# Kernel optimization log

Hardware: AMD Instinct MI355X
Metric: run time of the kernel (lower is better)

Reference implementation:

```python
import jax, jax.numpy as jnp
import numpy as np
from jax import lax

EPS = 1e-5

def quantize_ternary(w):
    # scale = mean(|w|).clamp_min(1e-5) computed on detached weight
    scale = jnp.maximum(jnp.mean(jnp.abs(lax.stop_gradient(w))), EPS)
    ws = w / scale
    # STE: forward uses round+clamp, backward is identity in ws
    wq = lax.stop_gradient(jnp.clip(jnp.round(ws), -1.0, 1.0) - ws) + ws
    return wq * scale

def conv2d(x, w, b):
    # x: [N,C,H,W], w: [O,I,kh,kw], stride 1, pad 1 -> same spatial size
    out = lax.conv_general_dilated(
        x, w, window_strides=(1, 1), padding=[(1, 1), (1, 1)],
        dimension_numbers=("NCHW", "OIHW", "NCHW"))
    return out + b[None, :, None, None]

def setup_inputs() -> dict:
    key = jax.random.key(0)
    k1, k2, k3, k4, k5 = jax.random.split(key, 5)
    N, C_in, C_out, H, W, K = 16, 64, 64, 128, 128, 3
    fan_in = C_in * K * K
    bound = 1.0 / np.sqrt(fan_in)
    x = jax.random.normal(k1, (N, C_in, H, W), dtype=jnp.float32)
    w = jax.random.uniform(k2, (C_out, C_in, K, K), minval=-bound, maxval=bound, dtype=jnp.float32)
    b = jax.random.uniform(k3, (C_out,), minval=-bound, maxval=bound, dtype=jnp.float32)
    # growth child: kaiming-uniform-like init scaled by 0.01, zero bias
    w_child = jax.random.uniform(k4, (C_out, C_in, K, K), minval=-bound, maxval=bound, dtype=jnp.float32) * 0.01
    b_child = jnp.zeros((C_out,), dtype=jnp.float32)
    gate = jnp.zeros((1,), dtype=jnp.float32)  # growth_gate buffer
    return {"x": x, "w": w, "b": b, "w_child": w_child, "b_child": b_child, "gate": gate}

def reference(x, w, b, w_child, b_child, gate):
    out = conv2d(x, quantize_ternary(w), b)
    child_out = conv2d(x, quantize_ternary(w_child), b_child)
    g = jax.nn.sigmoid(gate)  # shape [1], broadcasts
    return out + g * child_out
```

## Files before the change

### kernel.cpp

```cpp
#include <hip/hip_runtime.h>
#include <math.h>


typedef __attribute__((ext_vector_type(8))) short short8;
typedef __attribute__((ext_vector_type(4))) float float4v;

__device__ inline unsigned short f2bf(float f) {
  union { float f; unsigned u; } v; v.f = f;
  unsigned u = v.u;
  return (unsigned short)((u + 0x7FFFu + ((u >> 16) & 1u)) >> 16);
}

__global__ __launch_bounds__(1024) void reduce_abs_part(const float* __restrict__ w,
                                                        const float* __restrict__ wc,
                                                        double* __restrict__ part) {
  const int base = blockIdx.x * 4096 + threadIdx.x;
  double a = 0.0, c = 0.0;
#pragma unroll
  for (int i = 0; i < 4; ++i) {
    a += (double)fabsf(w[base + i * 1024]);
    c += (double)fabsf(wc[base + i * 1024]);
  }
#pragma unroll
  for (int off = 32; off > 0; off >>= 1) {
    a += __shfl_down(a, off);
    c += __shfl_down(c, off);
  }
  __shared__ double sa[16], sc[16];
  int wv = threadIdx.x >> 6;
  if ((threadIdx.x & 63) == 0) { sa[wv] = a; sc[wv] = c; }
  __syncthreads();
  if (threadIdx.x == 0) {
    double ta = 0.0, tc = 0.0;
#pragma unroll
    for (int i = 0; i < 16; ++i) { ta += sa[i]; tc += sc[i]; }
    part[blockIdx.x] = ta;
    part[9 + blockIdx.x] = tc;
  }
}

__global__ void quant_combine(const float* __restrict__ w, const float* __restrict__ wc,
                              const float* __restrict__ b, const float* __restrict__ bc,
                              const float* __restrict__ gate, const double* __restrict__ part,
                              unsigned short* __restrict__ wq, float* __restrict__ beff) {
  double s0 = 0.0, s1 = 0.0;
#pragma unroll
  for (int i = 0; i < 9; ++i) { s0 += part[i]; s1 += part[9 + i]; }
  const float sw = fmaxf((float)(s0 * (1.0 / 36864.0)), 1e-5f);
  const float sc = fmaxf((float)(s1 * (1.0 / 36864.0)), 1e-5f);
  const float g = 1.0f / (1.0f + expf(-gate[0]));
  int idx = blockIdx.x * 256 + threadIdx.x;
  int tap = idx >> 12;
  int oc = (idx >> 6) & 63;
  int ci = idx & 63;
  int src = oc * 576 + ci * 9 + tap;
  float q1 = fminf(1.f, fmaxf(-1.f, rintf(w[src] / sw))) * sw;
  float q2 = fminf(1.f, fmaxf(-1.f, rintf(wc[src] / sc))) * sc;
  wq[idx] = f2bf(q1 + g * q2);
  if (idx < 64) beff[idx] = b[idx] + g * bc[idx];
}

__global__ __launch_bounds__(512, 2) void conv_fused(
    const float* __restrict__ x, const unsigned short* __restrict__ wq,
    const float* __restrict__ beff, float* __restrict__ out) {
  extern __shared__ __align__(16) char smem[];
  char* Abase = smem;
  char* Bbase = smem + 99200;

  const int bid = blockIdx.x;
  const int xcd = bid & 7;
  const int u = bid >> 3;
  const int n = xcd * 2 + (u >> 5);
  const int h0 = (u & 31) * 4;
  const int tid = threadIdx.x;
  const int lane = tid & 63;
  const int wv = tid >> 6;
  const int rw = wv >> 1;
  const int pxh = (wv & 1) * 64;
  const int ln15 = lane & 15;
  const int lq = lane >> 4;

  const float* xn = x + (size_t)n * (64 * 16384);

  const short8 b0v = *(const short8*)(wq + tid * 8);

  if (tid < 56) {
    int slot = (tid < 48) ? ((tid >> 3) * 129 * 8 + (tid & 7)) : (6192 + (tid - 48));
    *(short8*)(Abase + (slot << 4)) = (short8)0;
  }

  const int w128 = tid & 127;
  const int hi = tid >> 7;
#pragma unroll 4
  for (int pass = 0; pass < 12; ++pass) {
    const int k = pass * 4 + hi;
    const int r = k >> 3;
    const int c = k & 7;
    const int h = h0 + r - 1;
    short8 v = (short8)0;
    if ((unsigned)h < 128u) {
      const float* sp = xn + c * 8 * 16384 + h * 128 + w128;
      v[0] = (short)f2bf(sp[0 * 16384]);
      v[1] = (short)f2bf(sp[1 * 16384]);
      v[2] = (short)f2bf(sp[2 * 16384]);
      v[3] = (short)f2bf(sp[3 * 16384]);
      v[4] = (short)f2bf(sp[4 * 16384]);
      v[5] = (short)f2bf(sp[5 * 16384]);
      v[6] = (short)f2bf(sp[6 * 16384]);
      v[7] = (short)f2bf(sp[7 * 16384]);
    }
    const int p = w128 + 1;
    const int slot = (r * 129 + p) * 8 + (c ^ (p & 7));
    *(short8*)(Abase + (slot << 4)) = v;
  }

  const int bslot = (tid & ~7) | ((tid & 7) ^ ((tid >> 3) & 7));
  *(short8*)(Bbase + (bslot << 4)) = b0v;
  __syncthreads();

  float4v acc[4][4] = {};

#pragma unroll
  for (int tap = 0; tap < 9; ++tap) {
    const int cb = tap & 1;
    short8 btrans;
    if (tap < 8) btrans = *(const short8*)(wq + (tap + 1) * 4096 + tid * 8);

    const int dh = tap / 3;
    const int dw = tap - dh * 3;
    const int r = rw + dh;
    const int pb = pxh + ln15 + dw;
    const int a0 = (((r * 129 + pb) << 3) + (lq ^ (pb & 7))) << 4;
    short8 Ab[2][4], Bb[2][4];
#pragma unroll
    for (int mf = 0; mf < 4; ++mf) {
      Ab[0][mf] = *(const short8*)(Abase + (a0 + mf * 2048));
      Ab[1][mf] = *(const short8*)(Abase + ((a0 ^ 64) + mf * 2048));
    }
#pragma unroll
    for (int qd = 0; qd < 4; ++qd) {
      const int oc = qd * 16 + ln15;
      Bb[0][qd] = *(const short8*)(Bbase + cb * 8192 +
                                   ((oc * 8 + (lq ^ (ln15 & 7))) << 4));
      Bb[1][qd] = *(const short8*)(Bbase + cb * 8192 +
                                   ((oc * 8 + ((lq + 4) ^ (ln15 & 7))) << 4));
    }

    __builtin_amdgcn_s_setprio(1);
#pragma unroll
    for (int cc2 = 0; cc2 < 2; ++cc2)
#pragma unroll
      for (int mf = 0; mf < 4; ++mf)
#pragma unroll
        for (int qd = 0; qd < 4; ++qd)
          acc[mf][qd] = __builtin_amdgcn_mfma_f32_16x16x32_bf16(
              Ab[cc2][mf], Bb[cc2][qd], acc[mf][qd], 0, 0, 0);
    __builtin_amdgcn_s_setprio(0);

    if (tap < 8) {
      *(short8*)(Bbase + (cb ^ 1) * 8192 + (bslot << 4)) = btrans;
      __syncthreads();
    }
  }

  const int rq = lane >> 4;
  float bias[4];
#pragma unroll
  for (int q = 0; q < 4; ++q) bias[q] = beff[q * 16 + ln15];
#pragma unroll
  for (int mf = 0; mf < 4; ++mf) {
#pragma unroll
    for (int qd = 0; qd < 4; ++qd) {
      float4v v = acc[mf][qd] + bias[qd];
      int oc = qd * 16 + ln15;
      float* op = out + (((n * 64 + oc) * 128 + h0 + rw) * 128 + pxh + mf * 16 + rq * 4);
      *(float4v*)op = v;
    }
  }
}

extern "C" void kernel_launch(void* const* d_in, const int* in_sizes, int n_in,
                              void* d_out, int out_size, void* d_ws, size_t ws_size,
                              hipStream_t stream) {
  const float* x = (const float*)d_in[0];
  const float* w = (const float*)d_in[1];
  const float* b = (const float*)d_in[2];
  const float* wc = (const float*)d_in[3];
  const float* bc = (const float*)d_in[4];
  const float* gate = (const float*)d_in[5];

  unsigned short* wq = (unsigned short*)d_ws;
  float* beff = (float*)((char*)d_ws + 73728);
  double* part = (double*)((char*)d_ws + 73984);

  reduce_abs_part<<<9, 1024, 0, stream>>>(w, wc, part);
  quant_combine<<<144, 256, 0, stream>>>(w, wc, b, bc, gate, part, wq, beff);
  conv_fused<<<512, 512, 115584, stream>>>(x, wq, beff, (float*)d_out);
}
```

Baseline: 144.0 us.

## Merge weight prep kernels and retile conv to two rows per block

Merges the abs-mean reduction and the quantize/combine step into one prep kernel, where every block recomputes the full reduction itself. This removes one launch and the partial-sum buffer. The conv kernel drops from 512 to 256 threads and from four to two output rows per block, doubling the grid to 1024 blocks. Its LDS falls to 80KB because the padded border columns are gone; edge pixels are now zeroed in registers with predicates. This trades a larger share of redundant halo-row loads and repeated per-block reduction work for smaller blocks that may fit two per CU.

```diff
diff --git a/kernel.cpp b/kernel.cpp
--- a/kernel.cpp
+++ b/kernel.cpp
@@ -11,67 +11,54 @@
   return (unsigned short)((u + 0x7FFFu + ((u >> 16) & 1u)) >> 16);
 }
 
-__global__ __launch_bounds__(1024) void reduce_abs_part(const float* __restrict__ w,
-                                                        const float* __restrict__ wc,
-                                                        double* __restrict__ part) {
-  const int base = blockIdx.x * 4096 + threadIdx.x;
+__global__ __launch_bounds__(256) void prep(
+    const float* __restrict__ w, const float* __restrict__ wc,
+    const float* __restrict__ b, const float* __restrict__ bc,
+    const float* __restrict__ gate,
+    unsigned short* __restrict__ wq, float* __restrict__ beff) {
+  const int tid = threadIdx.x;
   double a = 0.0, c = 0.0;
-#pragma unroll
-  for (int i = 0; i < 4; ++i) {
-    a += (double)fabsf(w[base + i * 1024]);
-    c += (double)fabsf(wc[base + i * 1024]);
+  for (int i = tid; i < 36864; i += 256) {
+    a += (double)fabsf(w[i]);
+    c += (double)fabsf(wc[i]);
   }
 #pragma unroll
   for (int off = 32; off > 0; off >>= 1) {
     a += __shfl_down(a, off);
     c += __shfl_down(c, off);
   }
-  __shared__ double sa[16], sc[16];
-  int wv = threadIdx.x >> 6;
-  if ((threadIdx.x & 63) == 0) { sa[wv] = a; sc[wv] = c; }
+  __shared__ double sa[4], sc[4];
+  const int wv = tid >> 6;
+  if ((tid & 63) == 0) { sa[wv] = a; sc[wv] = c; }
   __syncthreads();
-  if (threadIdx.x == 0) {
-    double ta = 0.0, tc = 0.0;
-#pragma unroll
-    for (int i = 0; i < 16; ++i) { ta += sa[i]; tc += sc[i]; }
-    part[blockIdx.x] = ta;
-    part[9 + blockIdx.x] = tc;
-  }
-}
-
-__global__ void quant_combine(const float* __restrict__ w, const float* __restrict__ wc,
-                              const float* __restrict__ b, const float* __restrict__ bc,
-                              const float* __restrict__ gate, const double* __restrict__ part,
-                              unsigned short* __restrict__ wq, float* __restrict__ beff) {
-  double s0 = 0.0, s1 = 0.0;
-#pragma unroll
-  for (int i = 0; i < 9; ++i) { s0 += part[i]; s1 += part[9 + i]; }
-  const float sw = fmaxf((float)(s0 * (1.0 / 36864.0)), 1e-5f);
-  const float sc = fmaxf((float)(s1 * (1.0 / 36864.0)), 1e-5f);
+  const double ta = sa[0] + sa[1] + sa[2] + sa[3];
+  const double tc = sc[0] + sc[1] + sc[2] + sc[3];
+  const float sw = fmaxf((float)(ta * (1.0 / 36864.0)), 1e-5f);
+  const float scl = fmaxf((float)(tc * (1.0 / 36864.0)), 1e-5f);
   const float g = 1.0f / (1.0f + expf(-gate[0]));
-  int idx = blockIdx.x * 256 + threadIdx.x;
-  int tap = idx >> 12;
-  int oc = (idx >> 6) & 63;
-  int ci = idx & 63;
-  int src = oc * 576 + ci * 9 + tap;
+  const int idx = blockIdx.x * 256 + tid;
+  const int tap = idx >> 12;
+  const int oc = (idx >> 6) & 63;
+  const int ci = idx & 63;
+  const int src = oc * 576 + ci * 9 + tap;
   float q1 = fminf(1.f, fmaxf(-1.f, rintf(w[src] / sw))) * sw;
-  float q2 = fminf(1.f, fmaxf(-1.f, rintf(wc[src] / sc))) * sc;
+  float q2 = fminf(1.f, fmaxf(-1.f, rintf(wc[src] / scl))) * scl;
   wq[idx] = f2bf(q1 + g * q2);
   if (idx < 64) beff[idx] = b[idx] + g * bc[idx];
 }
 
-__global__ __launch_bounds__(512, 2) void conv_fused(
+__global__ __launch_bounds__(256, 2) void conv_fused(
     const float* __restrict__ x, const unsigned short* __restrict__ wq,
     const float* __restrict__ beff, float* __restrict__ out) {
   extern __shared__ __align__(16) char smem[];
   char* Abase = smem;
-  char* Bbase = smem + 99200;
+  char* Bbase = smem + 65536;
 
   const int bid = blockIdx.x;
   const int xcd = bid & 7;
   const int u = bid >> 3;
-  const int n = xcd * 2 + (u >> 5);
-  const int h0 = (u & 31) * 4;
+  const int n = xcd * 2 + (u >> 6);
+  const int h0 = (u & 63) * 2;
   const int tid = threadIdx.x;
   const int lane = tid & 63;
   const int wv = tid >> 6;
@@ -82,24 +69,20 @@
 
   const float* xn = x + (size_t)n * (64 * 16384);
 
-  const short8 b0v = *(const short8*)(wq + tid * 8);
+  const short8 b0a = *(const short8*)(wq + tid * 16);
+  const short8 b0b = *(const short8*)(wq + tid * 16 + 8);
 
-  if (tid < 56) {
-    int slot = (tid < 48) ? ((tid >> 3) * 129 * 8 + (tid & 7)) : (6192 + (tid - 48));
-    *(short8*)(Abase + (slot << 4)) = (short8)0;
-  }
-
-  const int w128 = tid & 127;
+  const int pxc = tid & 127;
   const int hi = tid >> 7;
 #pragma unroll 4
-  for (int pass = 0; pass < 12; ++pass) {
-    const int k = pass * 4 + hi;
+  for (int pass = 0; pass < 16; ++pass) {
+    const int k = pass * 2 + hi;
     const int r = k >> 3;
     const int c = k & 7;
     const int h = h0 + r - 1;
     short8 v = (short8)0;
     if ((unsigned)h < 128u) {
-      const float* sp = xn + c * 8 * 16384 + h * 128 + w128;
+      const float* sp = xn + c * 8 * 16384 + h * 128 + pxc;
       v[0] = (short)f2bf(sp[0 * 16384]);
       v[1] = (short)f2bf(sp[1 * 16384]);
       v[2] = (short)f2bf(sp[2 * 16384]);
@@ -109,13 +92,17 @@
       v[6] = (short)f2bf(sp[6 * 16384]);
       v[7] = (short)f2bf(sp[7 * 16384]);
     }
-    const int p = w128 + 1;
-    const int slot = (r * 129 + p) * 8 + (c ^ (p & 7));
+    const int slot = ((r * 128 + pxc) << 3) + (c ^ ((pxc + 1) & 7));
     *(short8*)(Abase + (slot << 4)) = v;
   }
 
-  const int bslot = (tid & ~7) | ((tid & 7) ^ ((tid >> 3) & 7));
-  *(short8*)(Bbase + (bslot << 4)) = b0v;
+  const int g0 = tid * 2;
+  const int oc0 = g0 >> 3;
+  const int c0 = g0 & 7;
+  const int bs0 = (oc0 << 3) + (c0 ^ (oc0 & 7));
+  const int bs1 = (oc0 << 3) + ((c0 + 1) ^ (oc0 & 7));
+  *(short8*)(Bbase + (bs0 << 4)) = b0a;
+  *(short8*)(Bbase + (bs1 << 4)) = b0b;
   __syncthreads();
 
   float4v acc[4][4] = {};
@@ -123,27 +110,39 @@
 #pragma unroll
   for (int tap = 0; tap < 9; ++tap) {
     const int cb = tap & 1;
-    short8 btrans;
-    if (tap < 8) btrans = *(const short8*)(wq + (tap + 1) * 4096 + tid * 8);
+    short8 bta, btb;
+    if (tap < 8) {
+      bta = *(const short8*)(wq + (tap + 1) * 4096 + tid * 16);
+      btb = *(const short8*)(wq + (tap + 1) * 4096 + tid * 16 + 8);
+    }
 
     const int dh = tap / 3;
     const int dw = tap - dh * 3;
     const int r = rw + dh;
     const int pb = pxh + ln15 + dw;
-    const int a0 = (((r * 129 + pb) << 3) + (lq ^ (pb & 7))) << 4;
+    const bool p0 = (pb == 0);
+    const bool p129 = (pb == 81);
+    const int a0 = (((r * 128 + pb - 1) << 3) + (lq ^ (pb & 7))) << 4;
+    const int off0 = p0 ? 2048 : 0;
+    const int off3 = p129 ? 4096 : 6144;
+
     short8 Ab[2][4], Bb[2][4];
 #pragma unroll
-    for (int mf = 0; mf < 4; ++mf) {
-      Ab[0][mf] = *(const short8*)(Abase + (a0 + mf * 2048));
-      Ab[1][mf] = *(const short8*)(Abase + ((a0 ^ 64) + mf * 2048));
+    for (int cc = 0; cc < 2; ++cc) {
+      const int ax = a0 ^ (cc << 6);
+      Ab[cc][0] = *(const short8*)(Abase + (ax + off0));
+      Ab[cc][1] = *(const short8*)(Abase + (ax + 2048));
+      Ab[cc][2] = *(const short8*)(Abase + (ax + 4096));
+      Ab[cc][3] = *(const short8*)(Abase + (ax + off3));
+      if (p0) Ab[cc][0] = (short8)0;
+      if (p129) Ab[cc][3] = (short8)0;
     }
 #pragma unroll
     for (int qd = 0; qd < 4; ++qd) {
-      const int oc = qd * 16 + ln15;
-      Bb[0][qd] = *(const short8*)(Bbase + cb * 8192 +
-                                   ((oc * 8 + (lq ^ (ln15 & 7))) << 4));
-      Bb[1][qd] = *(const short8*)(Bbase + cb * 8192 +
-                                   ((oc * 8 + ((lq + 4) ^ (ln15 & 7))) << 4));
+      const int oc8 = ((qd << 4) + ln15) << 3;
+      const int k7 = ln15 & 7;
+      Bb[0][qd] = *(const short8*)(Bbase + (cb << 13) + ((oc8 + (lq ^ k7)) << 4));
+      Bb[1][qd] = *(const short8*)(Bbase + (cb << 13) + ((oc8 + ((lq + 4) ^ k7)) << 4));
     }
 
     __builtin_amdgcn_s_setprio(1);
@@ -158,7 +157,9 @@
     __builtin_amdgcn_s_setprio(0);
 
     if (tap < 8) {
-      *(short8*)(Bbase + (cb ^ 1) * 8192 + (bslot << 4)) = btrans;
+      char* bb = Bbase + ((cb ^ 1) << 13);
+      *(short8*)(bb + (bs0 << 4)) = bta;
+      *(short8*)(bb + (bs1 << 4)) = btb;
       __syncthreads();
     }
   }
@@ -191,9 +192,7 @@
 
   unsigned short* wq = (unsigned short*)d_ws;
   float* beff = (float*)((char*)d_ws + 73728);
-  double* part = (double*)((char*)d_ws + 73984);
 
-  reduce_abs_part<<<9, 1024, 0, stream>>>(w, wc, part);
-  quant_combine<<<144, 256, 0, stream>>>(w, wc, b, bc, gate, part, wq, beff);
-  conv_fused<<<512, 512, 115584, stream>>>(x, wq, beff, (float*)d_out);
+  prep<<<144, 256, 0, stream>>>(w, wc, b, bc, gate, wq, beff);
+  conv_fused<<<1024, 256, 81920, stream>>>(x, wq, beff, (float*)d_out);
 }
```

Result: slower. 183.9 us (+27.7%).
